# Optimization experiments

Hardware: AMD Instinct MI355X
Metric: run time of the kernel (lower is better)

The kernel has to match this reference:

```python
import jax, jax.numpy as jnp
import numpy as np

B, I, H = 16384, 1024, 1024

def setup_inputs() -> dict:
    key = jax.random.key(0)
    ks = jax.random.split(key, 7)
    scale = 0.02  # small init so gates are not saturated
    return {
        "x": jax.random.normal(ks[0], (B, I), jnp.float32),
        "h_prev": jax.random.normal(ks[1], (B, H), jnp.float32),
        "c_prev": jax.random.normal(ks[2], (B, H), jnp.float32),
        "Wx": jax.random.normal(ks[3], (4, H, I), jnp.float32) * scale,  # order: z,i,f,o
        "bx": jnp.zeros((4, H), jnp.float32),
        "Rh": jax.random.normal(ks[4], (4, H, H), jnp.float32) * scale,
        "bh": jnp.zeros((4, H), jnp.float32),
    }

def reference(x, h_prev, c_prev, Wx, bx, Rh, bh):
    # Fused form of 4 input-GEMMs + 4 recurrent-GEMMs: two einsums over stacked gates.
    # gate order g=0..3 -> z, i, f, o
    pre = (jnp.einsum('bi,ghi->bgh', x, Wx) + bx[None]
           + jnp.einsum('bh,gkh->bgk', h_prev, Rh) + bh[None])  # [B,4,H]
    z = jnp.tanh(pre[:, 0])
    i = jax.nn.sigmoid(pre[:, 1])
    f = jax.nn.sigmoid(pre[:, 2])
    o = jax.nn.sigmoid(pre[:, 3])
    c = f * c_prev + i * z
    h = o * jnp.tanh(c)
    return (h, c)
```

## Files before the change

kernel.cpp:

```cpp
#include <hip/hip_runtime.h>
#include <hip/hip_bf16.h>
#include <stdint.h>


typedef __attribute__((ext_vector_type(8))) short bf16x8;
typedef __attribute__((ext_vector_type(16))) float f32x16;
typedef __attribute__((ext_vector_type(8))) unsigned short u16x8;

#define AS1 __attribute__((address_space(1)))
#define AS3 __attribute__((address_space(3)))

constexpr int BATCH = 16384;
constexpr int HDIM  = 1024;
constexpr int KDIM  = 2048;
constexpr int NDIM  = 4096;

__device__ inline unsigned short f2bf(float f) {
  uint32_t u = __builtin_bit_cast(uint32_t, f);
  u += 0x7fffu + ((u >> 16) & 1u);
  return (unsigned short)(u >> 16);
}
__device__ inline u16x8 cvt8(const float* __restrict__ src) {
  float4 f0 = *(const float4*)src;
  float4 f1 = *(const float4*)(src + 4);
  u16x8 v;
  v[0] = f2bf(f0.x); v[1] = f2bf(f0.y); v[2] = f2bf(f0.z); v[3] = f2bf(f0.w);
  v[4] = f2bf(f1.x); v[5] = f2bf(f1.y); v[6] = f2bf(f1.z); v[7] = f2bf(f1.w);
  return v;
}
__device__ inline float sigmoid_f(float x) {
  float e = __builtin_amdgcn_exp2f(-1.4426950408889634f * x);
  return __builtin_amdgcn_rcpf(1.0f + e);
}
__device__ inline float tanh_f(float x) {
  float e = __builtin_amdgcn_exp2f(2.8853900817779268f * x);
  return 1.0f - 2.0f * __builtin_amdgcn_rcpf(1.0f + e);
}

__global__ void pack_xh(const float* __restrict__ x, const float* __restrict__ hp,
                        unsigned short* __restrict__ xh) {
  const int64_t nch = (int64_t)BATCH * KDIM / 8;
  for (int64_t c = (int64_t)blockIdx.x * blockDim.x + threadIdx.x; c < nch;
       c += (int64_t)gridDim.x * blockDim.x) {
    const int b = (int)(c >> 8);
    const int k = ((int)c & 255) * 8;
    const float* src = (k < 1024) ? (x + (int64_t)b * 1024 + k)
                                  : (hp + (int64_t)b * 1024 + (k - 1024));
    *(u16x8*)(xh + c * 8) = cvt8(src);
  }
}
__global__ void pack_w(const float* __restrict__ Wx, const float* __restrict__ Rh,
                       unsigned short* __restrict__ wp) {
  const int64_t nch = (int64_t)NDIM * KDIM / 8;
  for (int64_t c = (int64_t)blockIdx.x * blockDim.x + threadIdx.x; c < nch;
       c += (int64_t)gridDim.x * blockDim.x) {
    const int np = (int)(c >> 8);
    const int k = ((int)c & 255) * 8;
    const int h = np >> 2, g = np & 3;
    const float* src = (k < 1024) ? (Wx + (int64_t)(g * HDIM + h) * 1024 + k)
                                  : (Rh + (int64_t)(g * HDIM + h) * 1024 + (k - 1024));
    *(u16x8*)(wp + c * 8) = cvt8(src);
  }
}
__global__ void pack_bias(const float* __restrict__ bx, const float* __restrict__ bh,
                          float* __restrict__ bias) {
  int n = blockIdx.x * blockDim.x + threadIdx.x;
  if (n < NDIM) {
    int h = n >> 2, g = n & 3;
    bias[n] = bx[g * HDIM + h] + bh[g * HDIM + h];
  }
}

template <int OFF>
__device__ __forceinline__ bf16x8 dsb128(uint32_t a) {
  bf16x8 r;
  asm volatile("ds_read_b128 %0, %1 offset:%2" : "=v"(r) : "v"(a), "i"(OFF) : "memory");
  return r;
}

#define BARR   asm volatile("s_barrier" ::: "memory")
#define LGKM4  asm volatile("s_waitcnt lgkmcnt(4)" ::: "memory")
#define LGKM8  asm volatile("s_waitcnt lgkmcnt(8)" ::: "memory")
#define VM6    asm volatile("s_waitcnt vmcnt(6)" ::: "memory")
#define VM0    asm volatile("s_waitcnt vmcnt(0)" ::: "memory")
#define SCHED0 __builtin_amdgcn_sched_barrier(0)

#define ISS_A(FA, BUF, KH, MBH) { constexpr int _o = (BUF)*32768 + (KH)*16384 + (MBH)*4096; \
  FA[0] = dsb128<_o>(av0);      FA[1] = dsb128<_o>(av1);                                     \
  FA[2] = dsb128<_o+2048>(av0); FA[3] = dsb128<_o+2048>(av1); }
#define ISS_B(FB, BUF, KH) { constexpr int _o = (BUF)*32768 + (KH)*16384; \
  FB[0] = dsb128<_o>(bv0);      FB[1] = dsb128<_o>(bv1);                   \
  FB[2] = dsb128<_o+2048>(bv0); FB[3] = dsb128<_o+2048>(bv1); }

#define MFMA8(FA, FB, MBH) { \
  __builtin_amdgcn_s_setprio(1); \
  acc[(MBH)*2+0][0] = __builtin_amdgcn_mfma_f32_32x32x16_bf16(FA[0], FB[0], acc[(MBH)*2+0][0], 0, 0, 0); \
  acc[(MBH)*2+0][1] = __builtin_amdgcn_mfma_f32_32x32x16_bf16(FA[0], FB[2], acc[(MBH)*2+0][1], 0, 0, 0); \
  acc[(MBH)*2+1][0] = __builtin_amdgcn_mfma_f32_32x32x16_bf16(FA[2], FB[0], acc[(MBH)*2+1][0], 0, 0, 0); \
  acc[(MBH)*2+1][1] = __builtin_amdgcn_mfma_f32_32x32x16_bf16(FA[2], FB[2], acc[(MBH)*2+1][1], 0, 0, 0); \
  acc[(MBH)*2+0][0] = __builtin_amdgcn_mfma_f32_32x32x16_bf16(FA[1], FB[1], acc[(MBH)*2+0][0], 0, 0, 0); \
  acc[(MBH)*2+0][1] = __builtin_amdgcn_mfma_f32_32x32x16_bf16(FA[1], FB[3], acc[(MBH)*2+0][1], 0, 0, 0); \
  acc[(MBH)*2+1][0] = __builtin_amdgcn_mfma_f32_32x32x16_bf16(FA[3], FB[1], acc[(MBH)*2+1][0], 0, 0, 0); \
  acc[(MBH)*2+1][1] = __builtin_amdgcn_mfma_f32_32x32x16_bf16(FA[3], FB[3], acc[(MBH)*2+1][1], 0, 0, 0); \
  __builtin_amdgcn_s_setprio(0); }

#define STAGE(SRC, DOFF) { \
  __builtin_amdgcn_global_load_lds((const AS1 void*)(SRC), (AS3 void*)(dstL + (DOFF)), 16, 0, 0); \
  __builtin_amdgcn_global_load_lds((const AS1 void*)((SRC) + 524288), (AS3 void*)(dstL + (DOFF) + 8192), 16, 0, 0); }

__global__ __launch_bounds__(512, 2) void lstm_gemm(
    const unsigned short* __restrict__ XH, const unsigned short* __restrict__ Wp,
    const float* __restrict__ bias, const float* __restrict__ c_prev,
    float* __restrict__ out_h, float* __restrict__ out_c) {
  __shared__ __align__(1024) char smem_[131072];

  const int tid  = threadIdx.x;
  const int l    = tid & 63;
  const int w    = tid >> 6;
  const int wr   = w >> 2, wc = w & 3;

  const int xcd = blockIdx.x & 7;
  const int q   = blockIdx.x >> 3;
  const int tn  = xcd * 2 + (q & 1);
  const int tm  = q >> 1;
  const int m0  = tm * 256;
  const int n0  = tn * 256;

  const int rbase = w * 16 + (l >> 2);
  const int ck    = (l & 3) ^ ((l >> 3) & 3);
  const char* pA = (const char*)XH + (int64_t)(m0 + rbase) * 4096 + ck * 16;
  const char* pB = (const char*)Wp + (int64_t)(n0 + rbase) * 4096 + ck * 16;
  char* dstL = smem_ + w * 1024;

  const int r5  = l & 31;
  const int kh5 = l >> 5;
  const int qa0 = kh5 ^ ((r5 >> 1) & 3);
  const uint32_t lds0 = (uint32_t)(uintptr_t)(AS3 char*)smem_;
  const uint32_t av0 = lds0 + wr * 8192 + r5 * 64 + qa0 * 16;
  const uint32_t av1 = av0 ^ 32;
  const uint32_t bv0 = lds0 + 65536 + wc * 4096 + r5 * 64 + qa0 * 16;
  const uint32_t bv1 = bv0 ^ 32;

  f32x16 acc[4][2] = {};
  bf16x8 fa0[4], fa1[4], fb0[4], fb1[4];

  STAGE(pB,       65536);
  STAGE(pA,       0);
  STAGE(pB + 64,  81920);
  STAGE(pA + 64,  16384);
  STAGE(pB + 128, 98304);
  STAGE(pA + 128, 32768);
  STAGE(pB + 192, 114688);
  VM6; BARR;
  ISS_B(fb0, 0, 0) ISS_A(fa0, 0, 0, 0)

#pragma unroll 1
  for (int it = 0; it < 16; ++it) {
    int kt2 = 2 * it + 2; if (kt2 > 31) kt2 = 31;
    int kt3 = 2 * it + 3; if (kt3 > 31) kt3 = 31;
    const char* sA1 = pA + (2 * it + 1) * 128;
    const char* sA2 = pA + kt2 * 128;
    const char* sA3 = pA + kt3 * 128;
    const char* sB2 = pB + kt2 * 128;
    const char* sB3 = pB + kt3 * 128;

    BARR;
    STAGE(sA1 + 64, 49152);
    ISS_A(fa1, 0, 0, 1)
    LGKM4; SCHED0; MFMA8(fa0, fb0, 0)
    BARR;
    STAGE(sB2, 65536);
    ISS_B(fb1, 0, 1) ISS_A(fa0, 0, 1, 0)
    LGKM8; SCHED0; MFMA8(fa1, fb0, 1)
    VM6;
    BARR;
    STAGE(sA2, 0);
    ISS_A(fa1, 0, 1, 1)
    LGKM4; SCHED0; MFMA8(fa0, fb1, 0)
    BARR;
    STAGE(sB2 + 64, 81920);
    ISS_B(fb0, 1, 0) ISS_A(fa0, 1, 0, 0)
    LGKM8; SCHED0; MFMA8(fa1, fb1, 1)
    VM6;
    BARR;
    STAGE(sA2 + 64, 16384);
    ISS_A(fa1, 1, 0, 1)
    LGKM4; SCHED0; MFMA8(fa0, fb0, 0)
    BARR;
    STAGE(sB3, 98304);
    ISS_B(fb1, 1, 1) ISS_A(fa0, 1, 1, 0)
    LGKM8; SCHED0; MFMA8(fa1, fb0, 1)
    VM6;
    BARR;
    STAGE(sA3, 32768);
    ISS_A(fa1, 1, 1, 1)
    LGKM4; SCHED0; MFMA8(fa0, fb1, 0)
    BARR;
    STAGE(sB3 + 64, 114688);
    ISS_B(fb0, 0, 0) ISS_A(fa0, 0, 0, 0)
    LGKM8; SCHED0; MFMA8(fa1, fb1, 1)
    VM6;
  }

  VM0;
  __syncthreads();
  float* ew = (float*)smem_ + w * 2176;
  const float4 bias4 = *(const float4*)(bias + n0 + wc * 64 + 4 * (l & 15));
  const int hg = ((n0 + wc * 64) >> 2) + (l & 15);

#pragma unroll
  for (int mb = 0; mb < 4; ++mb) {
#pragma unroll
    for (int nb = 0; nb < 2; ++nb)
#pragma unroll
      for (int r = 0; r < 16; ++r)
        ew[((r & 3) + 8 * (r >> 2) + 4 * kh5) * 68 + nb * 32 + r5] = acc[mb][nb][r];
#pragma unroll
    for (int p = 0; p < 8; ++p) {
      const int row = p * 4 + (l >> 4);
      float4 g4 = *(const float4*)(ew + row * 68 + 4 * (l & 15));
      const int b = m0 + wr * 128 + mb * 32 + row;
      const uint32_t oidx = (uint32_t)b * HDIM + (uint32_t)hg;
      const float cp = c_prev[oidx];
      const float zg = tanh_f(g4.x + bias4.x);
      const float ig = sigmoid_f(g4.y + bias4.y);
      const float fg = sigmoid_f(g4.z + bias4.z);
      const float og = sigmoid_f(g4.w + bias4.w);
      const float cn = fg * cp + ig * zg;
      out_h[oidx] = og * tanh_f(cn);
      out_c[oidx] = cn;
    }
  }
}

extern "C" void kernel_launch(void* const* d_in, const int* in_sizes, int n_in,
                              void* d_out, int out_size, void* d_ws, size_t ws_size,
                              hipStream_t stream) {
  const float* x  = (const float*)d_in[0];
  const float* hp = (const float*)d_in[1];
  const float* cp = (const float*)d_in[2];
  const float* Wx = (const float*)d_in[3];
  const float* bx = (const float*)d_in[4];
  const float* Rh = (const float*)d_in[5];
  const float* bh = (const float*)d_in[6];

  unsigned short* XH = (unsigned short*)d_ws;
  unsigned short* Wp = XH + (size_t)BATCH * KDIM;
  float* bias = (float*)(Wp + (size_t)NDIM * KDIM);
  float* out_h = (float*)d_out;
  float* out_c = out_h + (size_t)BATCH * HDIM;

  pack_xh<<<2048, 256, 0, stream>>>(x, hp, XH);
  pack_w<<<1024, 256, 0, stream>>>(Wx, Rh, Wp);
  pack_bias<<<16, 256, 0, stream>>>(bx, bh, bias);
  lstm_gemm<<<1024, 512, 0, stream>>>(XH, Wp, bias, cp, out_h, out_c);
}
```

Baseline: 329.3 us.

## Merge pack kernels, change LDS swizzle, and prefetch c_prev before epilogue

Folds the three packing kernels (activations, weights, bias) into one launch, split by block index, to save two launch gaps. It also changes the XOR swizzle used for global-to-LDS staging and for the MFMA fragment reads, which is meant to cut LDS bank conflicts. The epilogue now loads all c_prev values into registers before the gate math so those global loads overlap. The register prefetch adds 32 floats per thread, and the new swizzle must match between the stage and read paths to stay correct.

```diff
diff --git a/kernel.cpp b/kernel.cpp
--- a/kernel.cpp
+++ b/kernel.cpp
@@ -37,37 +37,39 @@
   return 1.0f - 2.0f * __builtin_amdgcn_rcpf(1.0f + e);
 }
 
-__global__ void pack_xh(const float* __restrict__ x, const float* __restrict__ hp,
-                        unsigned short* __restrict__ xh) {
-  const int64_t nch = (int64_t)BATCH * KDIM / 8;
-  for (int64_t c = (int64_t)blockIdx.x * blockDim.x + threadIdx.x; c < nch;
-       c += (int64_t)gridDim.x * blockDim.x) {
-    const int b = (int)(c >> 8);
-    const int k = ((int)c & 255) * 8;
-    const float* src = (k < 1024) ? (x + (int64_t)b * 1024 + k)
-                                  : (hp + (int64_t)b * 1024 + (k - 1024));
-    *(u16x8*)(xh + c * 8) = cvt8(src);
-  }
-}
-__global__ void pack_w(const float* __restrict__ Wx, const float* __restrict__ Rh,
-                       unsigned short* __restrict__ wp) {
-  const int64_t nch = (int64_t)NDIM * KDIM / 8;
-  for (int64_t c = (int64_t)blockIdx.x * blockDim.x + threadIdx.x; c < nch;
-       c += (int64_t)gridDim.x * blockDim.x) {
-    const int np = (int)(c >> 8);
-    const int k = ((int)c & 255) * 8;
-    const int h = np >> 2, g = np & 3;
-    const float* src = (k < 1024) ? (Wx + (int64_t)(g * HDIM + h) * 1024 + k)
-                                  : (Rh + (int64_t)(g * HDIM + h) * 1024 + (k - 1024));
-    *(u16x8*)(wp + c * 8) = cvt8(src);
-  }
-}
-__global__ void pack_bias(const float* __restrict__ bx, const float* __restrict__ bh,
-                          float* __restrict__ bias) {
-  int n = blockIdx.x * blockDim.x + threadIdx.x;
-  if (n < NDIM) {
-    int h = n >> 2, g = n & 3;
-    bias[n] = bx[g * HDIM + h] + bh[g * HDIM + h];
+__global__ void pack_all(const float* __restrict__ x, const float* __restrict__ hp,
+                         const float* __restrict__ Wx, const float* __restrict__ Rh,
+                         const float* __restrict__ bx, const float* __restrict__ bh,
+                         unsigned short* __restrict__ xh, unsigned short* __restrict__ wp,
+                         float* __restrict__ bias) {
+  const int blk = blockIdx.x;
+  if (blk < 2048) {
+    const int64_t nch = (int64_t)BATCH * KDIM / 8;
+    for (int64_t c = (int64_t)blk * blockDim.x + threadIdx.x; c < nch;
+         c += (int64_t)2048 * blockDim.x) {
+      const int b = (int)(c >> 8);
+      const int k = ((int)c & 255) * 8;
+      const float* src = (k < 1024) ? (x + (int64_t)b * 1024 + k)
+                                    : (hp + (int64_t)b * 1024 + (k - 1024));
+      *(u16x8*)(xh + c * 8) = cvt8(src);
+    }
+  } else {
+    const int wblk = blk - 2048;
+    if (wblk < 16) {
+      const int n = wblk * 256 + threadIdx.x;
+      const int h = n >> 2, g = n & 3;
+      bias[n] = bx[g * HDIM + h] + bh[g * HDIM + h];
+    }
+    const int64_t nch = (int64_t)NDIM * KDIM / 8;
+    for (int64_t c = (int64_t)wblk * blockDim.x + threadIdx.x; c < nch;
+         c += (int64_t)1024 * blockDim.x) {
+      const int np = (int)(c >> 8);
+      const int k = ((int)c & 255) * 8;
+      const int h = np >> 2, g = np & 3;
+      const float* src = (k < 1024) ? (Wx + (int64_t)(g * HDIM + h) * 1024 + k)
+                                    : (Rh + (int64_t)(g * HDIM + h) * 1024 + (k - 1024));
+      *(u16x8*)(wp + c * 8) = cvt8(src);
+    }
   }
 }
 
@@ -127,14 +129,14 @@
   const int n0  = tn * 256;
 
   const int rbase = w * 16 + (l >> 2);
-  const int ck    = (l & 3) ^ ((l >> 3) & 3);
+  const int ck    = (l & 3) ^ ((l >> 2) & 3);
   const char* pA = (const char*)XH + (int64_t)(m0 + rbase) * 4096 + ck * 16;
   const char* pB = (const char*)Wp + (int64_t)(n0 + rbase) * 4096 + ck * 16;
   char* dstL = smem_ + w * 1024;
 
   const int r5  = l & 31;
   const int kh5 = l >> 5;
-  const int qa0 = kh5 ^ ((r5 >> 1) & 3);
+  const int qa0 = kh5 ^ (r5 & 3);
   const uint32_t lds0 = (uint32_t)(uintptr_t)(AS3 char*)smem_;
   const uint32_t av0 = lds0 + wr * 8192 + r5 * 64 + qa0 * 16;
   const uint32_t av1 = av0 ^ 32;
@@ -205,8 +207,17 @@
   VM0;
   __syncthreads();
   float* ew = (float*)smem_ + w * 2176;
-  const float4 bias4 = *(const float4*)(bias + n0 + wc * 64 + 4 * (l & 15));
-  const int hg = ((n0 + wc * 64) >> 2) + (l & 15);
+  const int la = l & 15;
+  const float4 bias4 = *(const float4*)(bias + n0 + wc * 64 + 4 * la);
+  const int hg = ((n0 + wc * 64) >> 2) + la;
+  const int brow0 = m0 + wr * 128;
+
+  float cpv[4][8];
+#pragma unroll
+  for (int mb = 0; mb < 4; ++mb)
+#pragma unroll
+    for (int p = 0; p < 8; ++p)
+      cpv[mb][p] = c_prev[(uint32_t)(brow0 + mb * 32 + p * 4 + (l >> 4)) * HDIM + (uint32_t)hg];
 
 #pragma unroll
   for (int mb = 0; mb < 4; ++mb) {
@@ -218,10 +229,10 @@
 #pragma unroll
     for (int p = 0; p < 8; ++p) {
       const int row = p * 4 + (l >> 4);
-      float4 g4 = *(const float4*)(ew + row * 68 + 4 * (l & 15));
-      const int b = m0 + wr * 128 + mb * 32 + row;
+      float4 g4 = *(const float4*)(ew + row * 68 + 4 * la);
+      const int b = brow0 + mb * 32 + row;
       const uint32_t oidx = (uint32_t)b * HDIM + (uint32_t)hg;
-      const float cp = c_prev[oidx];
+      const float cp = cpv[mb][p];
       const float zg = tanh_f(g4.x + bias4.x);
       const float ig = sigmoid_f(g4.y + bias4.y);
       const float fg = sigmoid_f(g4.z + bias4.z);
@@ -250,8 +261,6 @@
   float* out_h = (float*)d_out;
   float* out_c = out_h + (size_t)BATCH * HDIM;
 
-  pack_xh<<<2048, 256, 0, stream>>>(x, hp, XH);
-  pack_w<<<1024, 256, 0, stream>>>(Wx, Rh, Wp);
-  pack_bias<<<16, 256, 0, stream>>>(bx, bh, bias);
+  pack_all<<<3072, 256, 0, stream>>>(x, hp, Wx, Rh, bx, bh, XH, Wp, bias);
   lstm_gemm<<<1024, 512, 0, stream>>>(XH, Wp, bias, cp, out_h, out_c);
 }
```

Result: slower. 338.0 us (+2.6%).
